# Kernel optimization log

Hardware: AMD Instinct MI355X
Metric: run time of the kernel (lower is better)

## Reference

```python
import jax, jax.numpy as jnp
import numpy as np

B, T, C, NH = 1, 2048, 1024, 16
HS = C // NH            # 64
LEVEL = 6
LMIN = 2 ** LEVEL       # 64 (tail block size)
NB = T // LMIN          # 32 complete sets


def setup_inputs() -> dict:
    key = jax.random.key(0)
    ks = jax.random.split(key, 8)
    def w(k, shape, fan_in):
        return jax.random.normal(k, shape, jnp.float32) / np.sqrt(fan_in)
    return {
        "x": jax.random.normal(ks[0], (B, T, C), jnp.float32),
        "Wq": w(ks[1], (C, C), C),
        "Wk": w(ks[2], (C, C), C),
        "Wv": w(ks[3], (C, C), C),
        "Wkmap": w(ks[4], (HS, HS * HS), HS * HS),
        "bkmap": jnp.zeros((HS,), jnp.float32),
        "Wvmap": w(ks[5], (HS, HS * HS), HS * HS),
        "bvmap": jnp.zeros((HS,), jnp.float32),
        "Wc": w(ks[6], (C, C), C),
        "bc": jnp.zeros((C,), jnp.float32),
    }


def reference(x, Wq, Wk, Wv, Wkmap, bkmap, Wvmap, bvmap, Wc, bc):
    phi = lambda t: jax.nn.elu(t) + 1.0  # feature_map='elu'
    # preprocess: projections + feature map (no q/k normalization)
    q = phi((x @ Wq.T).reshape(B, T, NH, HS))
    k = phi((x @ Wk.T).reshape(B, T, NH, HS))
    v = (x @ Wv.T).reshape(B, T, NH, HS)

    # per-position outer products k_t (x) v_t, grouped into LMIN-sized blocks
    op = jnp.einsum('bthd,bthe->bthde', k, v).reshape(B, NB, LMIN, NH, HS, HS)
    # set feature = final state of linear-attn recurrence over each full block
    set_f = op.sum(axis=2).reshape(B, NB, NH, HS * HS)            # [B,NB,NH,HS^2]
    # tail feature at t = state over [t - t%LMIN, t] = in-block prefix cumsum
    tail_f = jnp.cumsum(op, axis=2).reshape(B, T, NH, HS * HS)    # [B,T,NH,HS^2]

    K = set_f @ Wkmap.T + bkmap      # [B,NB,NH,HS] (k_mapping=True)
    V = set_f @ Wvmap.T + bvmap      # [B,NB,NH,HS] (v_mapping=True)
    K_tail = tail_f @ Wkmap.T + bkmap  # [B,T,NH,HS]
    V_tail = tail_f @ Wvmap.T + bvmap  # [B,T,NH,HS]

    scale = 1.0 / np.sqrt(HS)
    logits = jnp.einsum('bthd,bshd->bhts', q, K) * scale          # [B,NH,T,NB]
    # query t may attend only complete sets strictly before its own block
    mask = jnp.arange(NB)[None, :] < (jnp.arange(T) // LMIN)[:, None]  # [T,NB]
    logits = jnp.where(mask[None, None], logits, -jnp.inf)
    tail_logit = (jnp.einsum('bthd,bthd->bth', q, K_tail) * scale)
    tail_logit = tail_logit.transpose(0, 2, 1)[..., None]         # [B,NH,T,1]

    att = jax.nn.softmax(jnp.concatenate([logits, tail_logit], axis=-1), axis=-1)
    out = (jnp.einsum('bhts,bshd->bhtd', att[..., :-1], V)
           + att[..., -1:] * V_tail.transpose(0, 2, 1, 3))        # [B,NH,T,HS]
    out = out.transpose(0, 2, 1, 3).reshape(B, T, C)
    return out @ Wc.T + bc
```

## Files before the change

kernel.cpp:

```cpp
#include <hip/hip_runtime.h>
#include <hip/hip_bf16.h>
#include <math.h>

typedef __hip_bfloat16 bf16;
typedef __attribute__((ext_vector_type(8))) short short8;
typedef __attribute__((ext_vector_type(4))) float f32x4;

#define C_DIM 1024
#define NHEAD 16
#define HS 64

__device__ __forceinline__ float bf2f(bf16 x) { return __bfloat162float(x); }

__device__ __forceinline__ void gl16(const void* g, void* l) {
    __builtin_amdgcn_global_load_lds(
        (const __attribute__((address_space(1))) unsigned int*)g,
        (__attribute__((address_space(3))) unsigned int*)l, 16, 0, 0);
}

__device__ __forceinline__ void split8(const float* p, short8& h, short8& l) {
    float4 f0 = reinterpret_cast<const float4*>(p)[0];
    float4 f1 = reinterpret_cast<const float4*>(p)[1];
    float vals[8] = {f0.x, f0.y, f0.z, f0.w, f1.x, f1.y, f1.z, f1.w};
#pragma unroll
    for (int j = 0; j < 8; ++j) {
        bf16 hb = __float2bfloat16(vals[j]);
        float r = vals[j] - __bfloat162float(hb);
        h[j] = *reinterpret_cast<short*>(&hb);
        bf16 lb = __float2bfloat16(r);
        l[j] = *reinterpret_cast<short*>(&lb);
    }
}

__device__ __forceinline__ short8* tchunk(bf16* tile, int row, int ch) {
    return reinterpret_cast<short8*>(tile + row * 64 + (((ch) ^ (row & 7)) << 3));
}

__global__ __launch_bounds__(256) void presplit_all_kernel(
    const float* __restrict__ x, const float* __restrict__ Wq,
    const float* __restrict__ Wk, const float* __restrict__ Wv,
    bf16* __restrict__ xh, bf16* __restrict__ xl,
    bf16* __restrict__ wqh, bf16* __restrict__ wql,
    bf16* __restrict__ wkh, bf16* __restrict__ wkl,
    bf16* __restrict__ wvh, bf16* __restrict__ wvl)
{
    int blk = blockIdx.x;
    const float* src; bf16 *dh, *dl; long off;
    if (blk < 1024)      { src = x;  dh = xh;  dl = xl;  off = (long)blk * 2048; }
    else if (blk < 1536) { src = Wq; dh = wqh; dl = wql; off = (long)(blk - 1024) * 2048; }
    else if (blk < 2048) { src = Wk; dh = wkh; dl = wkl; off = (long)(blk - 1536) * 2048; }
    else                 { src = Wv; dh = wvh; dl = wvl; off = (long)(blk - 2048) * 2048; }
    long p = off + threadIdx.x * 8;
    int j = (int)(((p >> 3) ^ (p >> 10)) & 7);
    long dp = (p & ~56l) | ((long)j << 3);
    short8 h8, l8;
    split8(&src[p], h8, l8);
    *reinterpret_cast<short8*>(&dh[dp]) = h8;
    *reinterpret_cast<short8*>(&dl[dp]) = l8;
}

__global__ __launch_bounds__(256) void presplit_wc_kernel(
    const float* __restrict__ Wc, bf16* __restrict__ wch, bf16* __restrict__ wcl)
{
    long p = (long)blockIdx.x * 2048 + threadIdx.x * 8;
    int j = (int)(((p >> 3) ^ (p >> 10)) & 7);
    long dp = (p & ~56l) | ((long)j << 3);
    short8 h8, l8;
    split8(&Wc[p], h8, l8);
    *reinterpret_cast<short8*>(&wch[dp]) = h8;
    *reinterpret_cast<short8*>(&wcl[dp]) = l8;
}

__global__ __launch_bounds__(256) void presplit_wmap_kernel(
    const float* __restrict__ WK, const float* __restrict__ WV, bf16* __restrict__ Wm4)
{
    int d = blockIdx.x;
    int row = threadIdx.x >> 2, e0 = (threadIdx.x & 3) * 16;
    int sw0 = (((e0 >> 3) + 0) ^ (row & 7)) & 7;
    int sw1 = (((e0 >> 3) + 1) ^ (row & 7)) & 7;
    const float* pk = &WK[(long)row * 4096 + d * 64 + e0];
    const float* pv = &WV[(long)row * 4096 + d * 64 + e0];
    long bKh = ((long)(d * 4 + 0) * 64 + row) * 64;
    long bKl = ((long)(d * 4 + 1) * 64 + row) * 64;
    long bVh = ((long)(d * 4 + 2) * 64 + row) * 64;
    long bVl = ((long)(d * 4 + 3) * 64 + row) * 64;
    short8 h8, l8;
    split8(pk, h8, l8);     *(short8*)&Wm4[bKh + sw0*8] = h8; *(short8*)&Wm4[bKl + sw0*8] = l8;
    split8(pk + 8, h8, l8); *(short8*)&Wm4[bKh + sw1*8] = h8; *(short8*)&Wm4[bKl + sw1*8] = l8;
    split8(pv, h8, l8);     *(short8*)&Wm4[bVh + sw0*8] = h8; *(short8*)&Wm4[bVl + sw0*8] = l8;
    split8(pv + 8, h8, l8); *(short8*)&Wm4[bVh + sw1*8] = h8; *(short8*)&Wm4[bVl + sw1*8] = l8;
}

__global__ __launch_bounds__(256) void qkv_kernel(
    const bf16* __restrict__ xh, const bf16* __restrict__ xl,
    const bf16* __restrict__ wqh, const bf16* __restrict__ wql,
    const bf16* __restrict__ wkh, const bf16* __restrict__ wkl,
    const bf16* __restrict__ wvh, const bf16* __restrict__ wvl,
    float* __restrict__ qkv)
{
    __shared__ bf16 lds[32768];
    const int tid = threadIdx.x;
    const int lane = tid & 63, wid = tid >> 6;
    const int wr = wid >> 1, wc = wid & 1;
    const int proj = blockIdx.x >> 3;
    const int n0 = (blockIdx.x & 7) * 128;
    const int m0 = blockIdx.y * 128;
    const bf16* Bhp = proj == 0 ? wqh : (proj == 1 ? wkh : wvh);
    const bf16* Blp = proj == 0 ? wql : (proj == 1 ? wkl : wvl);
    float* C = qkv + (long)proj * 2097152;
    char* lb = reinterpret_cast<char*>(lds);

    f32x4 acc[4][4] = {};
    for (int kt = 0; kt < 16; ++kt) {
        const int k0 = kt << 6;
#pragma unroll
        for (int i = 0; i < 4; ++i) {
            int cc = tid + i * 256;
            int row = cc >> 3, j = cc & 7;
            long soA = (long)(m0 + row) * 1024 + k0 + j * 8;
            long soB = (long)(n0 + row) * 1024 + k0 + j * 8;
            gl16(&xh[soA],  lb + cc * 16);
            gl16(&xl[soA],  lb + 16384 + cc * 16);
            gl16(&Bhp[soB], lb + 32768 + cc * 16);
            gl16(&Blp[soB], lb + 49152 + cc * 16);
        }
        __syncthreads();
#pragma unroll
        for (int kk = 0; kk < 2; ++kk) {
            short8 afh[4], afl[4], bfh[4], bfl[4];
#pragma unroll
            for (int t = 0; t < 4; ++t) {
                int ra = wr * 64 + t * 16 + (lane & 15);
                int rb = wc * 64 + t * 16 + (lane & 15);
                int ch = kk * 4 + (lane >> 4);
                afh[t] = *tchunk(lds, ra, ch);
                afl[t] = *tchunk(lds + 8192, ra, ch);
                bfh[t] = *tchunk(lds + 16384, rb, ch);
                bfl[t] = *tchunk(lds + 24576, rb, ch);
            }
#pragma unroll
            for (int tm = 0; tm < 4; ++tm)
#pragma unroll
                for (int tn = 0; tn < 4; ++tn) {
                    acc[tm][tn] = __builtin_amdgcn_mfma_f32_16x16x32_bf16(
                        afh[tm], bfh[tn], acc[tm][tn], 0, 0, 0);
                    acc[tm][tn] = __builtin_amdgcn_mfma_f32_16x16x32_bf16(
                        afh[tm], bfl[tn], acc[tm][tn], 0, 0, 0);
                    acc[tm][tn] = __builtin_amdgcn_mfma_f32_16x16x32_bf16(
                        afl[tm], bfh[tn], acc[tm][tn], 0, 0, 0);
                }
        }
        __syncthreads();
    }
#pragma unroll
    for (int tm = 0; tm < 4; ++tm)
#pragma unroll
        for (int tn = 0; tn < 4; ++tn)
#pragma unroll
            for (int r = 0; r < 4; ++r) {
                int row = m0 + wr * 64 + tm * 16 + (lane >> 4) * 4 + r;
                int col = n0 + wc * 64 + tn * 16 + (lane & 15);
                float v = acc[tm][tn][r];
                if (proj < 2) v = v > 0.f ? v + 1.f : __expf(v);
                C[(long)row * 1024 + col] = v;
            }
}

__global__ __launch_bounds__(512) void setfeat_kernel(
    const float* __restrict__ kbuf, const float* __restrict__ vbuf,
    const bf16* __restrict__ Wm4,
    const float* __restrict__ bkmap, const float* __restrict__ bvmap,
    float* __restrict__ Ktail, float* __restrict__ Vtail,
    float* __restrict__ Kset, float* __restrict__ Vset)
{
    __shared__ char smem[65536];
    bf16* Wt = reinterpret_cast<bf16*>(smem);
    const int tid = threadIdx.x;
    const int grp = tid >> 8;
    const int tl = tid & 255;
    const int lane = tl & 63, wid = tl >> 6;
    const int wr = wid >> 1, wc = wid & 1;
    const int pairIdx = blockIdx.x * 2 + grp;
    const int b = pairIdx >> 4, h = pairIdx & 15;
    const long base_kv = ((long)b * 64) * C_DIM + h * HS;
    float* kT = reinterpret_cast<float*>(smem + 32768 + grp * 16384);

    {
        int s = tl >> 2, cg = tl & 3;
        const float* src = &kbuf[base_kv + (long)s * C_DIM + cg * 16];
        float f[16];
#pragma unroll
        for (int j = 0; j < 4; ++j)
            *reinterpret_cast<float4*>(&f[j * 4]) = reinterpret_cast<const float4*>(src)[j];
#pragma unroll
        for (int j = 0; j < 16; ++j)
            kT[(cg * 16 + j) * 64 + s] = f[j];
    }
    short8 vh[2][2], vl[2][2];
#pragma unroll
    for (int tm = 0; tm < 2; ++tm)
#pragma unroll
        for (int kk = 0; kk < 2; ++kk) {
            const float* vp = &vbuf[base_kv +
                (long)(wr * 32 + tm * 16 + (lane & 15)) * C_DIM + kk * 32 + (lane >> 4) * 8];
            split8(vp, vh[tm][kk], vl[tm][kk]);
        }
    f32x4 accK[2][2] = {}, accV[2][2] = {};
    __syncthreads();

    for (int d = 0; d < 64; ++d) {
#pragma unroll
        for (int i = 0; i < 4; ++i) {
            int cc = tid + i * 512;
            gl16(&Wm4[(long)d * 16384 + (long)cc * 8], smem + (long)cc * 16);
        }
        __syncthreads();
        f32x4 GK[2][2] = {}, GV[2][2] = {};
#pragma unroll
        for (int kk = 0; kk < 2; ++kk) {
            short8 bkh[2], bkl[2], bvh[2], bvl[2];
#pragma unroll
            for (int t = 0; t < 2; ++t) {
                int rb = wc * 32 + t * 16 + (lane & 15);
                int ch = kk * 4 + (lane >> 4);
                bkh[t] = *tchunk(Wt,         rb, ch);
                bkl[t] = *tchunk(Wt + 4096,  rb, ch);
                bvh[t] = *tchunk(Wt + 8192,  rb, ch);
                bvl[t] = *tchunk(Wt + 12288, rb, ch);
            }
#pragma unroll
            for (int tm = 0; tm < 2; ++tm)
#pragma unroll
                for (int tn = 0; tn < 2; ++tn) {
                    GK[tm][tn] = __builtin_amdgcn_mfma_f32_16x16x32_bf16(
                        vh[tm][kk], bkh[tn], GK[tm][tn], 0, 0, 0);
                    GK[tm][tn] = __builtin_amdgcn_mfma_f32_16x16x32_bf16(
                        vh[tm][kk], bkl[tn], GK[tm][tn], 0, 0, 0);
                    GK[tm][tn] = __builtin_amdgcn_mfma_f32_16x16x32_bf16(
                        vl[tm][kk], bkh[tn], GK[tm][tn], 0, 0, 0);
                    GV[tm][tn] = __builtin_amdgcn_mfma_f32_16x16x32_bf16(
                        vh[tm][kk], bvh[tn], GV[tm][tn], 0, 0, 0);
                    GV[tm][tn] = __builtin_amdgcn_mfma_f32_16x16x32_bf16(
                        vh[tm][kk], bvl[tn], GV[tm][tn], 0, 0, 0);
                    GV[tm][tn] = __builtin_amdgcn_mfma_f32_16x16x32_bf16(
                        vl[tm][kk], bvh[tn], GV[tm][tn], 0, 0, 0);
                }
        }
#pragma unroll
        for (int tm = 0; tm < 2; ++tm) {
            f32x4 kv = *reinterpret_cast<const f32x4*>(
                &kT[d * 64 + wr * 32 + tm * 16 + (lane >> 4) * 4]);
#pragma unroll
            for (int tn = 0; tn < 2; ++tn)
#pragma unroll
                for (int r = 0; r < 4; ++r) {
                    accK[tm][tn][r] += kv[r] * GK[tm][tn][r];
                    accV[tm][tn][r] += kv[r] * GV[tm][tn][r];
                }
        }
        __syncthreads();
    }
    float(*WallK)[64] = reinterpret_cast<float(*)[64]>(smem + grp * 32768);
    float(*WallV)[64] = reinterpret_cast<float(*)[64]>(smem + grp * 32768 + 16384);
#pragma unroll
    for (int tm = 0; tm < 2; ++tm)
#pragma unroll
        for (int tn = 0; tn < 2; ++tn)
#pragma unroll
            for (int r = 0; r < 4; ++r) {
                int row = wr * 32 + tm * 16 + (lane >> 4) * 4 + r;
                int col = wc * 32 + tn * 16 + (lane & 15);
                WallK[row][col] = accK[tm][tn][r];
                WallV[row][col] = accV[tm][tn][r];
            }
    __syncthreads();
    if (tl < 128) {
        int i = tl & 63;
        bool isV = tl >= 64;
        const float bi = isV ? bvmap[i] : bkmap[i];
        float run = 0.f;
        for (int s = 0; s < 64; ++s) {
            run += isV ? WallV[s][i] : WallK[s][i];
            float val = run + bi;
            long t = (long)b * 64 + s;
            if (isV) Vtail[t * C_DIM + h * HS + i] = val;
            else     Ktail[t * C_DIM + h * HS + i] = val;
            if (s == 63) {
                if (isV) Vset[(b * NHEAD + h) * HS + i] = val;
                else     Kset[(b * NHEAD + h) * HS + i] = val;
            }
        }
    }
}

__global__ __launch_bounds__(256) void attn_kernel(
    const float* __restrict__ qbuf, const float* __restrict__ Kset,
    const float* __restrict__ Vset, const float* __restrict__ Ktail,
    const float* __restrict__ Vtail, bf16* __restrict__ atth, bf16* __restrict__ attl)
{
    __shared__ float qsh[4][64];
    __shared__ float attsh[4][64];
    const int tid = threadIdx.x, lane = tid & 63, wid = tid >> 6;
    const int g = blockIdx.x * 4 + wid;
    const int t = g >> 4, h = g & 15;
    const int nb = t >> 6;
    const float scale = 0.125f;
    const long qoff = (long)t * C_DIM + h * HS;
    qsh[wid][lane] = qbuf[qoff + lane];
    __syncthreads();
    float logit = -INFINITY;
    if (lane < nb) {
        float s = 0.f;
        const float* Kp = &Kset[(lane * NHEAD + h) * HS];
        for (int d = 0; d < 64; ++d) s += qsh[wid][d] * Kp[d];
        logit = s * scale;
    } else if (lane == nb) {
        float s = 0.f;
        const float* Kp = &Ktail[qoff];
        for (int d = 0; d < 64; ++d) s += qsh[wid][d] * Kp[d];
        logit = s * scale;
    }
    float m = logit;
    for (int off = 32; off; off >>= 1) m = fmaxf(m, __shfl_xor(m, off, 64));
    float e = (lane <= nb) ? __expf(logit - m) : 0.f;
    float sum = e;
    for (int off = 32; off; off >>= 1) sum += __shfl_xor(sum, off, 64);
    attsh[wid][lane] = e / sum;
    __syncthreads();
    float out = 0.f;
    for (int s = 0; s < nb; ++s)
        out += attsh[wid][s] * Vset[(s * NHEAD + h) * HS + lane];
    out += attsh[wid][nb] * Vtail[qoff + lane];
    bf16 hb = __float2bfloat16(out);
    int csw = (((lane >> 3) ^ (t & 7)) << 3) | (lane & 7);
    long po = (long)t * 1024 + h * 64 + csw;
    atth[po] = hb;
    attl[po] = __float2bfloat16(out - bf2f(hb));
}

__global__ __launch_bounds__(256) void gemm_final_kernel(
    const bf16* __restrict__ ah, const bf16* __restrict__ al,
    const bf16* __restrict__ bh, const bf16* __restrict__ bl,
    const float* __restrict__ bias, float* __restrict__ C)
{
    __shared__ bf16 lds[24576];
    const int tid = threadIdx.x;
    const int lane = tid & 63, wid = tid >> 6;
    const int wr = wid >> 1, wc = wid & 1;
    const int m0 = blockIdx.y * 128, n0 = blockIdx.x * 64;
    char* lb = reinterpret_cast<char*>(lds);

    f32x4 acc[4][2] = {};
    for (int kt = 0; kt < 16; ++kt) {
        const int k0 = kt << 6;
#pragma unroll
        for (int i = 0; i < 4; ++i) {
            int cc = tid + i * 256;
            int row = cc >> 3, j = cc & 7;
            long so = (long)(m0 + row) * 1024 + k0 + j * 8;
            gl16(&ah[so], lb + cc * 16);
            gl16(&al[so], lb + 16384 + cc * 16);
        }
#pragma unroll
        for (int i = 0; i < 2; ++i) {
            int cc = tid + i * 256;
            int row = cc >> 3, j = cc & 7;
            long so = (long)(n0 + row) * 1024 + k0 + j * 8;
            gl16(&bh[so], lb + 32768 + cc * 16);
            gl16(&bl[so], lb + 40960 + cc * 16);
        }
        __syncthreads();
#pragma unroll
        for (int kk = 0; kk < 2; ++kk) {
            short8 afh[4], afl[4], bfh[2], bfl[2];
#pragma unroll
            for (int t = 0; t < 4; ++t) {
                int ra = wr * 64 + t * 16 + (lane & 15);
                int ch = kk * 4 + (lane >> 4);
                afh[t] = *tchunk(lds, ra, ch);
                afl[t] = *tchunk(lds + 8192, ra, ch);
            }
#pragma unroll
            for (int t = 0; t < 2; ++t) {
                int rb = wc * 32 + t * 16 + (lane & 15);
                int ch = kk * 4 + (lane >> 4);
                bfh[t] = *tchunk(lds + 16384, rb, ch);
                bfl[t] = *tchunk(lds + 20480, rb, ch);
            }
#pragma unroll
            for (int tm = 0; tm < 4; ++tm)
#pragma unroll
                for (int tn = 0; tn < 2; ++tn) {
                    acc[tm][tn] = __builtin_amdgcn_mfma_f32_16x16x32_bf16(
                        afh[tm], bfh[tn], acc[tm][tn], 0, 0, 0);
                    acc[tm][tn] = __builtin_amdgcn_mfma_f32_16x16x32_bf16(
                        afh[tm], bfl[tn], acc[tm][tn], 0, 0, 0);
                    acc[tm][tn] = __builtin_amdgcn_mfma_f32_16x16x32_bf16(
                        afl[tm], bfh[tn], acc[tm][tn], 0, 0, 0);
                }
        }
        __syncthreads();
    }
#pragma unroll
    for (int tm = 0; tm < 4; ++tm)
#pragma unroll
        for (int tn = 0; tn < 2; ++tn)
#pragma unroll
            for (int r = 0; r < 4; ++r) {
                int row = m0 + wr * 64 + tm * 16 + (lane >> 4) * 4 + r;
                int col = n0 + wc * 32 + tn * 16 + (lane & 15);
                C[(long)row * 1024 + col] = acc[tm][tn][r] + bias[col];
            }
}

extern "C" void kernel_launch(void* const* d_in, const int* in_sizes, int n_in,
                              void* d_out, int out_size, void* d_ws, size_t ws_size,
                              hipStream_t stream)
{
    const float* x     = (const float*)d_in[0];
    const float* Wq    = (const float*)d_in[1];
    const float* Wk    = (const float*)d_in[2];
    const float* Wv    = (const float*)d_in[3];
    const float* Wkmap = (const float*)d_in[4];
    const float* bkmap = (const float*)d_in[5];
    const float* Wvmap = (const float*)d_in[6];
    const float* bvmap = (const float*)d_in[7];
    const float* Wc    = (const float*)d_in[8];
    const float* bc    = (const float*)d_in[9];
    float* out = (float*)d_out;

    char* ws = (char*)d_ws;
    const long MB = 1l << 20;
    float* q   = (float*)(ws + 0 * MB);
    float* k   = (float*)(ws + 8 * MB);
    float* v   = (float*)(ws + 16 * MB);
    bf16* xh   = (bf16*)(ws + 24 * MB);
    bf16* xl   = (bf16*)(ws + 28 * MB);
    bf16* wqh  = (bf16*)(ws + 32 * MB);
    bf16* wql  = (bf16*)(ws + 34 * MB);
    bf16* wkh  = (bf16*)(ws + 36 * MB);
    bf16* wkl  = (bf16*)(ws + 38 * MB);
    bf16* wvh  = (bf16*)(ws + 40 * MB);
    bf16* wvl  = (bf16*)(ws + 42 * MB);
    bf16* Wm4  = (bf16*)(ws + 44 * MB);
    float* Ktail = (float*)(ws + 24 * MB);
    float* Vtail = (float*)(ws + 32 * MB);
    float* Kset  = (float*)(ws + 40 * MB);
    float* Vset  = (float*)(ws + 41 * MB);
    bf16* atth   = (bf16*)(ws + 8 * MB);
    bf16* attl   = (bf16*)(ws + 12 * MB);
    bf16* wch    = (bf16*)(ws + 44 * MB);
    bf16* wcl    = (bf16*)(ws + 46 * MB);

    presplit_all_kernel<<<2560, 256, 0, stream>>>(x, Wq, Wk, Wv, xh, xl,
                                                  wqh, wql, wkh, wkl, wvh, wvl);
    presplit_wmap_kernel<<<64, 256, 0, stream>>>(Wkmap, Wvmap, Wm4);
    qkv_kernel<<<dim3(24, 16), 256, 0, stream>>>(xh, xl, wqh, wql, wkh, wkl,
                                                 wvh, wvl, q);
    setfeat_kernel<<<256, 512, 0, stream>>>(k, v, Wm4, bkmap, bvmap,
                                            Ktail, Vtail, Kset, Vset);
    presplit_wc_kernel<<<512, 256, 0, stream>>>(Wc, wch, wcl);
    attn_kernel<<<8192, 256, 0, stream>>>(q, Kset, Vset, Ktail, Vtail, atth, attl);
    gemm_final_kernel<<<dim3(16, 16), 256, 0, stream>>>(atth, attl, wch, wcl, bc, out);
}
```

Measured before the change: 292.2 us.

## Double-buffer Wmap tiles in setfeat and transpose Kset for coalesced attention reads

setfeat now keeps two LDS buffers for the Wmap slice. It issues the async global-to-LDS load for slice d+1 while computing on slice d, which removes the load-then-barrier stall at the top of each iteration. The set keys are written in a [head][dim][block] layout, so attention lanes that each handle a different block read adjacent addresses instead of 256-byte-strided ones. The tail logit is now a lane-parallel product plus a wave shuffle reduction instead of a serial 64-step loop in one lane. LDS use grows from 64KB to 96KB per block, which may lower occupancy.

New measurement: 266.2 us. 8.9% less time.

```diff
diff --git a/kernel.cpp b/kernel.cpp
--- a/kernel.cpp
+++ b/kernel.cpp
@@ -171,10 +171,11 @@
     const bf16* __restrict__ Wm4,
     const float* __restrict__ bkmap, const float* __restrict__ bvmap,
     float* __restrict__ Ktail, float* __restrict__ Vtail,
-    float* __restrict__ Kset, float* __restrict__ Vset)
-{
-    __shared__ char smem[65536];
-    bf16* Wt = reinterpret_cast<bf16*>(smem);
+    float* __restrict__ KsetT, float* __restrict__ Vset)
+{
+    __shared__ char smem[98304];
+    bf16* W0 = reinterpret_cast<bf16*>(smem);
+    bf16* W1 = reinterpret_cast<bf16*>(smem + 32768);
     const int tid = threadIdx.x;
     const int grp = tid >> 8;
     const int tl = tid & 255;
@@ -183,7 +184,7 @@
     const int pairIdx = blockIdx.x * 2 + grp;
     const int b = pairIdx >> 4, h = pairIdx & 15;
     const long base_kv = ((long)b * 64) * C_DIM + h * HS;
-    float* kT = reinterpret_cast<float*>(smem + 32768 + grp * 16384);
+    float* kT = reinterpret_cast<float*>(smem + 65536 + grp * 16384);
 
     {
         int s = tl >> 2, cg = tl & 3;
@@ -205,16 +206,24 @@
                 (long)(wr * 32 + tm * 16 + (lane & 15)) * C_DIM + kk * 32 + (lane >> 4) * 8];
             split8(vp, vh[tm][kk], vl[tm][kk]);
         }
+#pragma unroll
+    for (int i = 0; i < 4; ++i) {
+        int cc = tid + i * 512;
+        gl16(&Wm4[(long)cc * 8], smem + (long)cc * 16);
+    }
     f32x4 accK[2][2] = {}, accV[2][2] = {};
     __syncthreads();
 
     for (int d = 0; d < 64; ++d) {
-#pragma unroll
-        for (int i = 0; i < 4; ++i) {
-            int cc = tid + i * 512;
-            gl16(&Wm4[(long)d * 16384 + (long)cc * 8], smem + (long)cc * 16);
-        }
-        __syncthreads();
+        bf16* Wcur = (d & 1) ? W1 : W0;
+        char* Wnxt = (d & 1) ? smem : smem + 32768;
+        if (d < 63) {
+#pragma unroll
+            for (int i = 0; i < 4; ++i) {
+                int cc = tid + i * 512;
+                gl16(&Wm4[(long)(d + 1) * 16384 + (long)cc * 8], Wnxt + (long)cc * 16);
+            }
+        }
         f32x4 GK[2][2] = {}, GV[2][2] = {};
 #pragma unroll
         for (int kk = 0; kk < 2; ++kk) {
@@ -223,10 +232,10 @@
             for (int t = 0; t < 2; ++t) {
                 int rb = wc * 32 + t * 16 + (lane & 15);
                 int ch = kk * 4 + (lane >> 4);
-                bkh[t] = *tchunk(Wt,         rb, ch);
-                bkl[t] = *tchunk(Wt + 4096,  rb, ch);
-                bvh[t] = *tchunk(Wt + 8192,  rb, ch);
-                bvl[t] = *tchunk(Wt + 12288, rb, ch);
+                bkh[t] = *tchunk(Wcur,         rb, ch);
+                bkl[t] = *tchunk(Wcur + 4096,  rb, ch);
+                bvh[t] = *tchunk(Wcur + 8192,  rb, ch);
+                bvl[t] = *tchunk(Wcur + 12288, rb, ch);
             }
 #pragma unroll
             for (int tm = 0; tm < 2; ++tm)
@@ -287,14 +296,14 @@
             else     Ktail[t * C_DIM + h * HS + i] = val;
             if (s == 63) {
                 if (isV) Vset[(b * NHEAD + h) * HS + i] = val;
-                else     Kset[(b * NHEAD + h) * HS + i] = val;
+                else     KsetT[h * 2048 + i * 32 + b] = val;
             }
         }
     }
 }
 
 __global__ __launch_bounds__(256) void attn_kernel(
-    const float* __restrict__ qbuf, const float* __restrict__ Kset,
+    const float* __restrict__ qbuf, const float* __restrict__ KsetT,
     const float* __restrict__ Vset, const float* __restrict__ Ktail,
     const float* __restrict__ Vtail, bf16* __restrict__ atth, bf16* __restrict__ attl)
 {
@@ -306,19 +315,19 @@
     const int nb = t >> 6;
     const float scale = 0.125f;
     const long qoff = (long)t * C_DIM + h * HS;
-    qsh[wid][lane] = qbuf[qoff + lane];
+    float qv = qbuf[qoff + lane];
+    qsh[wid][lane] = qv;
+    float tp = qv * Ktail[qoff + lane];
+    for (int off = 32; off; off >>= 1) tp += __shfl_xor(tp, off, 64);
     __syncthreads();
     float logit = -INFINITY;
     if (lane < nb) {
         float s = 0.f;
-        const float* Kp = &Kset[(lane * NHEAD + h) * HS];
-        for (int d = 0; d < 64; ++d) s += qsh[wid][d] * Kp[d];
+        const float* Kp = &KsetT[h * 2048 + lane];
+        for (int d = 0; d < 64; ++d) s += qsh[wid][d] * Kp[d * 32];
         logit = s * scale;
     } else if (lane == nb) {
-        float s = 0.f;
-        const float* Kp = &Ktail[qoff];
-        for (int d = 0; d < 64; ++d) s += qsh[wid][d] * Kp[d];
-        logit = s * scale;
+        logit = tp * scale;
     }
     float m = logit;
     for (int off = 32; off; off >>= 1) m = fmaxf(m, __shfl_xor(m, off, 64));
@@ -445,7 +454,7 @@
     bf16* Wm4  = (bf16*)(ws + 44 * MB);
     float* Ktail = (float*)(ws + 24 * MB);
     float* Vtail = (float*)(ws + 32 * MB);
-    float* Kset  = (float*)(ws + 40 * MB);
+    float* KsetT = (float*)(ws + 40 * MB);
     float* Vset  = (float*)(ws + 41 * MB);
     bf16* atth   = (bf16*)(ws + 8 * MB);
     bf16* attl   = (bf16*)(ws + 12 * MB);
@@ -458,8 +467,8 @@
     qkv_kernel<<<dim3(24, 16), 256, 0, stream>>>(xh, xl, wqh, wql, wkh, wkl,
                                                  wvh, wvl, q);
     setfeat_kernel<<<256, 512, 0, stream>>>(k, v, Wm4, bkmap, bvmap,
-                                            Ktail, Vtail, Kset, Vset);
+                                            Ktail, Vtail, KsetT, Vset);
     presplit_wc_kernel<<<512, 256, 0, stream>>>(Wc, wch, wcl);
-    attn_kernel<<<8192, 256, 0, stream>>>(q, Kset, Vset, Ktail, Vtail, atth, attl);
+    attn_kernel<<<8192, 256, 0, stream>>>(q, KsetT, Vset, Ktail, Vtail, atth, attl);
     gemm_final_kernel<<<dim3(16, 16), 256, 0, stream>>>(atth, attl, wch, wcl, bc, out);
 }
```
